# Kernel optimization log

Measured on AMD Instinct MI355X. Metric: run time of the kernel, lower is better.

Reference implementation:

```python
import jax, jax.numpy as jnp
import numpy as np

B, N, ENC, DEC, E, ATT, V, T = 64, 196, 2048, 512, 512, 512, 32000, 32


def setup_inputs() -> dict:
    key = jax.random.key(0)
    ks = jax.random.split(key, 12)
    s = 0.02  # param init scale
    f = lambda k, shape: jax.random.normal(k, shape, jnp.float32) * s
    return {
        "features": jax.random.normal(ks[0], (B, N, ENC), jnp.float32),
        "captions": jax.random.randint(ks[1], (B, T), 0, V),
        "emb": f(ks[2], (V, E)),
        "att_Wenc": f(ks[3], (ENC, ATT)),
        "att_Wdec": f(ks[4], (DEC, ATT)),
        "att_v": f(ks[5], (ATT,)),
        "init_h_W": f(ks[6], (ENC, DEC)), "init_h_b": jnp.zeros((DEC,), jnp.float32),
        "init_c_W": f(ks[7], (ENC, DEC)), "init_c_b": jnp.zeros((DEC,), jnp.float32),
        "W_ih": f(ks[8], (4 * DEC, E + ENC)), "W_hh": f(ks[9], (4 * DEC, DEC)),
        "b_ih": jnp.zeros((4 * DEC,), jnp.float32), "b_hh": jnp.zeros((4 * DEC,), jnp.float32),
        "out_W": f(ks[10], (DEC, V)), "out_b": jnp.zeros((V,), jnp.float32),
    }


def reference(features, captions, emb, att_Wenc, att_Wdec, att_v,
              init_h_W, init_h_b, init_c_W, init_c_b,
              W_ih, W_hh, b_ih, b_hh, out_W, out_b):
    # init hidden/cell from mean-pooled encoder features
    mean_f = features.mean(axis=1)                      # [B, ENC]
    h = mean_f @ init_h_W + init_h_b                    # [B, DEC]
    c = mean_f @ init_c_W + init_c_b                    # [B, DEC]

    enc_att = features @ att_Wenc                       # [B, N, ATT] (loop-invariant)
    embs = emb[captions]                                # [B, T, E]
    xs = jnp.swapaxes(embs[:, :-1], 0, 1)               # [T-1, B, E] time-major

    def step(carry, x):
        h, c = carry
        # Bahdanau attention: tanh(Wf + Wh) . v -> softmax over spatial locations
        e = jnp.tanh(enc_att + (h @ att_Wdec)[:, None, :]) @ att_v   # [B, N]
        alpha = jax.nn.softmax(e, axis=1)                            # [B, N]
        context = jnp.einsum('bn,bnd->bd', alpha, features)          # [B, ENC]
        lstm_in = jnp.concatenate([x, context], axis=1)              # [B, E+ENC]
        gates = lstm_in @ W_ih.T + b_ih + h @ W_hh.T + b_hh          # [B, 4*DEC]
        i, f, g, o = jnp.split(gates, 4, axis=1)                     # torch gate order
        c = jax.nn.sigmoid(f) * c + jax.nn.sigmoid(i) * jnp.tanh(g)
        h = jax.nn.sigmoid(o) * jnp.tanh(c)
        out = h @ out_W + out_b                                      # dropout = identity (eval)
        return (h, c), (out, alpha)

    _, (preds, alphas) = jax.lax.scan(step, (h, c), xs)
    # back to batch-major: preds [B, T-1, V], alphas [B, T-1, N]
    return jnp.swapaxes(preds, 0, 1), jnp.swapaxes(alphas, 0, 1)
```

## Files before the change

kernel.cpp:

```cpp
#include <hip/hip_runtime.h>
#include <math.h>

constexpr int kB = 64, kN = 196, kENC = 2048, kDEC = 512, kE = 512, kATT = 512;
constexpr int kV = 32000, kT = 32, kTS = 31;
constexpr int kKIH = kE + kENC;
constexpr int kKC  = kKIH + kDEC;
constexpr int kG   = 4 * kDEC;
constexpr int kSPL = 8, kKSP = kKC / kSPL;

typedef __attribute__((ext_vector_type(8))) short bf8;
typedef __attribute__((ext_vector_type(4))) float f4;

__device__ __forceinline__ f4 mfma16(bf8 a, bf8 b, f4 c){
  asm("v_mfma_f32_16x16x32_bf16 %0, %1, %2, %0" : "+v"(c) : "v"(a), "v"(b));
  return c;
}
__device__ __forceinline__ float bf2f(unsigned short u){
  return __uint_as_float(((unsigned)u) << 16);
}
__device__ __forceinline__ unsigned short f2b(float f){
  unsigned u = __float_as_uint(f);
  u += 0x7fffu + ((u >> 16) & 1u);
  return (unsigned short)(u >> 16);
}
__device__ __forceinline__ float th_(float x){
  float e2 = __expf(2.f * x);
  return 1.f - 2.f * __builtin_amdgcn_rcpf(e2 + 1.f);
}
__device__ __forceinline__ float sg_(float x){
  return __builtin_amdgcn_rcpf(1.f + __expf(-x));
}

__global__ void k_cvt(const float* __restrict__ src, unsigned short* __restrict__ dst, int n8){
  int i = blockIdx.x * 256 + threadIdx.x;
  if (i >= n8) return;
  float4 a = ((const float4*)src)[2 * i];
  float4 b = ((const float4*)src)[2 * i + 1];
  union { unsigned short u[8]; uint4 v; } t;
  t.u[0] = f2b(a.x); t.u[1] = f2b(a.y); t.u[2] = f2b(a.z); t.u[3] = f2b(a.w);
  t.u[4] = f2b(b.x); t.u[5] = f2b(b.y); t.u[6] = f2b(b.z); t.u[7] = f2b(b.w);
  ((uint4*)dst)[i] = t.v;
}

__global__ __launch_bounds__(256) void k_tcvt(const float* __restrict__ src,
                                              unsigned short* __restrict__ dst, int R, int C){
  __shared__ float t[32][33];
  int c0 = blockIdx.x * 32, r0 = blockIdx.y * 32;
  int tx = threadIdx.x & 31, ty = threadIdx.x >> 5;
  #pragma unroll
  for (int j = 0; j < 4; j++)
    t[ty + 8*j][tx] = src[(size_t)(r0 + ty + 8*j) * C + c0 + tx];
  __syncthreads();
  #pragma unroll
  for (int j = 0; j < 4; j++)
    dst[(size_t)(c0 + ty + 8*j) * R + r0 + tx] = f2b(t[tx][ty + 8*j]);
}

__global__ void k_mean(const float* __restrict__ feat, float* __restrict__ meanf){
  int b = blockIdx.x, d = blockIdx.y * 256 + threadIdx.x;
  const float* p = feat + (size_t)b * kN * kENC + d;
  float s = 0.f;
  for (int n = 0; n < kN; n++) s += p[(size_t)n * kENC];
  meanf[b * kENC + d] = s * (1.f / kN);
}

__global__ __launch_bounds__(512) void k_init(const float* __restrict__ meanf,
                       const float* __restrict__ Wh, const float* __restrict__ bh,
                       const float* __restrict__ Wc, const float* __restrict__ bc,
                       float* __restrict__ h, float* __restrict__ c){
  __shared__ float mf[kENC];
  int b = blockIdx.x;
  for (int i = threadIdx.x; i < kENC; i += 512) mf[i] = meanf[b * kENC + i];
  __syncthreads();
  int j = threadIdx.x;
  const float* W  = blockIdx.y ? Wc : Wh;
  const float* bb = blockIdx.y ? bc : bh;
  float acc = bb[j];
  for (int k = 0; k < kENC; k++) acc = fmaf(mf[k], W[k * kDEC + j], acc);
  (blockIdx.y ? c : h)[b * kDEC + j] = acc;
}

__global__ __launch_bounds__(256) void k_encatt(const unsigned short* __restrict__ A,
                                                const unsigned short* __restrict__ Bt,
                                                unsigned short* __restrict__ Cb){
  int w = threadIdx.x >> 6, lane = threadIdx.x & 63;
  int m0 = blockIdx.x * 128 + w * 32, n0 = blockIdx.y * 64;
  int lr = lane & 15, lk = (lane >> 4) * 8;
  f4 acc[2][4] = {};
  const unsigned short* Ap = A  + (size_t)(m0 + lr) * kENC + lk;
  const unsigned short* Bp = Bt + (size_t)(n0 + lr) * kENC + lk;
  for (int k0 = 0; k0 < kENC; k0 += 32){
    bf8 a0 = *(const bf8*)(Ap + k0);
    bf8 a1 = *(const bf8*)(Ap + 16 * kENC + k0);
    bf8 b0 = *(const bf8*)(Bp + k0);
    bf8 b1 = *(const bf8*)(Bp + 16 * kENC + k0);
    bf8 b2 = *(const bf8*)(Bp + 32 * kENC + k0);
    bf8 b3 = *(const bf8*)(Bp + 48 * kENC + k0);
    acc[0][0] = mfma16(a0, b0, acc[0][0]); acc[0][1] = mfma16(a0, b1, acc[0][1]);
    acc[0][2] = mfma16(a0, b2, acc[0][2]); acc[0][3] = mfma16(a0, b3, acc[0][3]);
    acc[1][0] = mfma16(a1, b0, acc[1][0]); acc[1][1] = mfma16(a1, b1, acc[1][1]);
    acc[1][2] = mfma16(a1, b2, acc[1][2]); acc[1][3] = mfma16(a1, b3, acc[1][3]);
  }
  asm volatile("s_nop 7\n\ts_nop 7");
  int orow = (lane >> 4) * 4;
  #pragma unroll
  for (int mt = 0; mt < 2; mt++)
    #pragma unroll
    for (int nt = 0; nt < 4; nt++)
      #pragma unroll
      for (int r = 0; r < 4; r++)
        Cb[(size_t)(m0 + mt*16 + orow + r) * kATT + n0 + nt*16 + lr] = f2b(acc[mt][nt][r]);
}

__global__ __launch_bounds__(256) void k_e(const unsigned short* __restrict__ EA,
                   const float* __restrict__ hWdec,
                   const float* __restrict__ attv, float* __restrict__ e){
  int w = threadIdx.x >> 6, lane = threadIdx.x & 63;
  int r = blockIdx.x * 4 + w;
  int b = r / kN;
  bf8 ev = *(const bf8*)(EA + (size_t)r * kATT + lane * 8);
  const float* hw = hWdec + b * kATT + lane * 8;
  const float* av = attv + lane * 8;
  float4 h0 = *(const float4*)hw, h1 = *(const float4*)(hw + 4);
  float4 v0 = *(const float4*)av, v1 = *(const float4*)(av + 4);
  float s = 0.f;
  s = fmaf(th_(bf2f((unsigned short)ev[0]) + h0.x), v0.x, s);
  s = fmaf(th_(bf2f((unsigned short)ev[1]) + h0.y), v0.y, s);
  s = fmaf(th_(bf2f((unsigned short)ev[2]) + h0.z), v0.z, s);
  s = fmaf(th_(bf2f((unsigned short)ev[3]) + h0.w), v0.w, s);
  s = fmaf(th_(bf2f((unsigned short)ev[4]) + h1.x), v1.x, s);
  s = fmaf(th_(bf2f((unsigned short)ev[5]) + h1.y), v1.y, s);
  s = fmaf(th_(bf2f((unsigned short)ev[6]) + h1.z), v1.z, s);
  s = fmaf(th_(bf2f((unsigned short)ev[7]) + h1.w), v1.w, s);
  #pragma unroll
  for (int off = 32; off; off >>= 1) s += __shfl_xor(s, off, 64);
  if (lane == 0) e[r] = s;
}

__global__ __launch_bounds__(256) void k_ctx(const float* __restrict__ e,
                     const unsigned short* __restrict__ featb,
                     unsigned short* __restrict__ Xb, float* __restrict__ alphas, int t){
  __shared__ float al[kN];
  __shared__ float red[256];
  int b = blockIdx.x, tid = threadIdx.x;
  float ev = (tid < kN) ? e[b * kN + tid] : -1e30f;
  red[tid] = ev; __syncthreads();
  for (int off = 128; off; off >>= 1){ if (tid < off) red[tid] = fmaxf(red[tid], red[tid + off]); __syncthreads(); }
  float mx = red[0]; __syncthreads();
  float ex = (tid < kN) ? __expf(ev - mx) : 0.f;
  red[tid] = ex; __syncthreads();
  for (int off = 128; off; off >>= 1){ if (tid < off) red[tid] += red[tid + off]; __syncthreads(); }
  float inv = 1.f / red[0];
  if (tid < kN){
    float a = ex * inv;
    al[tid] = a;
    if (blockIdx.y == 0) alphas[((size_t)b * kTS + t) * kN + tid] = a;
  }
  __syncthreads();
  int d = blockIdx.y * 512 + tid * 2;
  const unsigned short* fp = featb + (size_t)b * kN * kENC + d;
  float c0 = 0.f, c1 = 0.f;
  #pragma unroll 4
  for (int n = 0; n < kN; n++){
    unsigned u = *(const unsigned*)(fp + (size_t)n * kENC);
    float a = al[n];
    c0 = fmaf(bf2f((unsigned short)(u & 0xffffu)), a, c0);
    c1 = fmaf(bf2f((unsigned short)(u >> 16)), a, c1);
  }
  unsigned o = ((unsigned)f2b(c1) << 16) | (unsigned)f2b(c0);
  *(unsigned*)(Xb + (size_t)b * kKC + kE + d) = o;
}

__global__ __launch_bounds__(256) void k_gates(const unsigned short* __restrict__ X,
        const unsigned short* __restrict__ Wih, const unsigned short* __restrict__ Whh,
        float* __restrict__ gpart){
  int w = threadIdx.x >> 6, lane = threadIdx.x & 63;
  int n0 = blockIdx.x * 64 + w * 16, ks = blockIdx.y;
  int lr = lane & 15, lk = (lane >> 4) * 8;
  int nrow = n0 + lr;
  f4 acc[4] = {};
  const unsigned short* Xp = X + (size_t)lr * kKC + lk;
  for (int kt = 0; kt < kKSP; kt += 32){
    int kk = ks * kKSP + kt + lk;
    bf8 a0 = *(const bf8*)(Xp + ks * kKSP + kt);
    bf8 a1 = *(const bf8*)(Xp + 16 * kKC + ks * kKSP + kt);
    bf8 a2 = *(const bf8*)(Xp + 32 * kKC + ks * kKSP + kt);
    bf8 a3 = *(const bf8*)(Xp + 48 * kKC + ks * kKSP + kt);
    const unsigned short* bp = (kk < kKIH) ? (Wih + (size_t)nrow * kKIH + kk)
                                           : (Whh + (size_t)nrow * kDEC + (kk - kKIH));
    bf8 b = *(const bf8*)bp;
    acc[0] = mfma16(a0, b, acc[0]); acc[1] = mfma16(a1, b, acc[1]);
    acc[2] = mfma16(a2, b, acc[2]); acc[3] = mfma16(a3, b, acc[3]);
  }
  asm volatile("s_nop 7\n\ts_nop 7");
  float* gp = gpart + (size_t)ks * kB * kG;
  int orow = (lane >> 4) * 4;
  #pragma unroll
  for (int mt = 0; mt < 4; mt++)
    #pragma unroll
    for (int r = 0; r < 4; r++)
      gp[(size_t)(mt*16 + orow + r) * kG + n0 + lr] = acc[mt][r];
}

__global__ __launch_bounds__(512) void k_lstm(const float* __restrict__ gpart,
      const float* __restrict__ bih, const float* __restrict__ bhh,
      float* __restrict__ c, unsigned short* __restrict__ Xb,
      const float* __restrict__ emb, const int* __restrict__ captions,
      const float* __restrict__ Wdec, float* __restrict__ hWdec, int tnext){
  __shared__ float hl[kDEC];
  int b = blockIdx.x, d = threadIdx.x;
  float gi = 0.f, gf = 0.f, gg = 0.f, go = 0.f;
  for (int ks = 0; ks < kSPL; ks++){
    const float* gp = gpart + ((size_t)ks * kB + b) * kG;
    gi += gp[d]; gf += gp[kDEC + d]; gg += gp[2*kDEC + d]; go += gp[3*kDEC + d];
  }
  gi += bih[d]          + bhh[d];
  gf += bih[kDEC + d]   + bhh[kDEC + d];
  gg += bih[2*kDEC + d] + bhh[2*kDEC + d];
  go += bih[3*kDEC + d] + bhh[3*kDEC + d];
  float cn = sg_(gf) * c[b*kDEC + d] + sg_(gi) * th_(gg);
  float hn = sg_(go) * th_(cn);
  c[b*kDEC + d] = cn;
  hl[d] = hn;
  Xb[(size_t)b * kKC + kKIH + d] = f2b(hn);
  Xb[(size_t)b * kKC + d] = f2b(emb[(size_t)captions[b*kT + tnext] * kE + d]);
  __syncthreads();
  float a = 0.f;
  for (int k = 0; k < kDEC; k++) a = fmaf(hl[k], Wdec[(size_t)k * kATT + d], a);
  hWdec[b * kATT + d] = a;
}

__global__ __launch_bounds__(512) void k_prep(const float* __restrict__ h0,
      unsigned short* __restrict__ Xb, const float* __restrict__ emb,
      const int* __restrict__ captions,
      const float* __restrict__ Wdec, float* __restrict__ hWdec){
  __shared__ float hl[kDEC];
  int b = blockIdx.x, d = threadIdx.x;
  float hv = h0[b*kDEC + d];
  hl[d] = hv;
  Xb[(size_t)b * kKC + kKIH + d] = f2b(hv);
  Xb[(size_t)b * kKC + d] = f2b(emb[(size_t)captions[b*kT] * kE + d]);
  __syncthreads();
  float a = 0.f;
  for (int k = 0; k < kDEC; k++) a = fmaf(hl[k], Wdec[(size_t)k * kATT + d], a);
  hWdec[b * kATT + d] = a;
}

__global__ __launch_bounds__(256) void k_out(const unsigned short* __restrict__ Xh,
        const unsigned short* __restrict__ Wt,
        const float* __restrict__ bias, float* __restrict__ preds, int t){
  int w = threadIdx.x >> 6, lane = threadIdx.x & 63;
  int n0 = blockIdx.x * 64 + w * 16;
  int lr = lane & 15, lk = (lane >> 4) * 8;
  float bv = bias[n0 + lr];
  f4 bvv = {bv, bv, bv, bv};
  f4 acc[4] = {bvv, bvv, bvv, bvv};
  const unsigned short* Wp = Wt + (size_t)(n0 + lr) * kDEC + lk;
  const unsigned short* Xp = Xh + (size_t)lr * kKC + lk;
  for (int k0 = 0; k0 < kDEC; k0 += 32){
    bf8 b  = *(const bf8*)(Wp + k0);
    bf8 a0 = *(const bf8*)(Xp + k0);
    bf8 a1 = *(const bf8*)(Xp + 16 * kKC + k0);
    bf8 a2 = *(const bf8*)(Xp + 32 * kKC + k0);
    bf8 a3 = *(const bf8*)(Xp + 48 * kKC + k0);
    acc[0] = mfma16(a0, b, acc[0]); acc[1] = mfma16(a1, b, acc[1]);
    acc[2] = mfma16(a2, b, acc[2]); acc[3] = mfma16(a3, b, acc[3]);
  }
  asm volatile("s_nop 7\n\ts_nop 7");
  int orow = (lane >> 4) * 4;
  #pragma unroll
  for (int mt = 0; mt < 4; mt++)
    #pragma unroll
    for (int r = 0; r < 4; r++){
      int bb = mt*16 + orow + r;
      preds[((size_t)bb * kTS + t) * kV + n0 + lr] = acc[mt][r];
    }
}

extern "C" void kernel_launch(void* const* d_in, const int* in_sizes, int n_in,
                              void* d_out, int out_size, void* d_ws, size_t ws_size,
                              hipStream_t stream) {
  const float* feat     = (const float*)d_in[0];
  const int*   captions = (const int*)  d_in[1];
  const float* emb      = (const float*)d_in[2];
  const float* attWenc  = (const float*)d_in[3];
  const float* attWdec  = (const float*)d_in[4];
  const float* attv     = (const float*)d_in[5];
  const float* ihW      = (const float*)d_in[6];
  const float* ihb      = (const float*)d_in[7];
  const float* icW      = (const float*)d_in[8];
  const float* icb      = (const float*)d_in[9];
  const float* Wih      = (const float*)d_in[10];
  const float* Whh      = (const float*)d_in[11];
  const float* bih      = (const float*)d_in[12];
  const float* bhh      = (const float*)d_in[13];
  const float* outW     = (const float*)d_in[14];
  const float* outb     = (const float*)d_in[15];

  float* preds  = (float*)d_out;
  float* alphas = preds + (size_t)kB * kTS * kV;

  char* p = (char*)d_ws;
  unsigned short* featb  = (unsigned short*)p; p += (size_t)kB*kN*kENC*2;
  unsigned short* outWb  = (unsigned short*)p; p += (size_t)kV*kDEC*2;
  unsigned short* Wihb   = (unsigned short*)p; p += (size_t)kG*kKIH*2;
  unsigned short* Whhb   = (unsigned short*)p; p += (size_t)kG*kDEC*2;
  unsigned short* attWT  = (unsigned short*)p; p += (size_t)kATT*kENC*2;
  unsigned short* encattb= (unsigned short*)p; p += (size_t)kB*kN*kATT*2;
  unsigned short* Xb     = (unsigned short*)p; p += (size_t)kB*kKC*2;
  float* gpart = (float*)p; p += (size_t)kSPL*kB*kG*4;
  float* meanf = (float*)p; p += (size_t)kB*kENC*4;
  float* h0    = (float*)p; p += (size_t)kB*kDEC*4;
  float* cbuf  = (float*)p; p += (size_t)kB*kDEC*4;
  float* hWdec = (float*)p; p += (size_t)kB*kATT*4;
  float* evec  = (float*)p; p += (size_t)kB*kN*4;

  k_cvt<<<(kB*kN*kENC/8 + 255)/256, 256, 0, stream>>>(feat, featb, kB*kN*kENC/8);
  k_cvt<<<(kG*kKIH/8 + 255)/256, 256, 0, stream>>>(Wih, Wihb, kG*kKIH/8);
  k_cvt<<<(kG*kDEC/8 + 255)/256, 256, 0, stream>>>(Whh, Whhb, kG*kDEC/8);
  k_tcvt<<<dim3(kATT/32, kENC/32), 256, 0, stream>>>(attWenc, attWT, kENC, kATT);
  k_tcvt<<<dim3(kV/32, kDEC/32), 256, 0, stream>>>(outW, outWb, kDEC, kV);

  k_mean<<<dim3(kB, kENC/256), 256, 0, stream>>>(feat, meanf);
  k_init<<<dim3(kB, 2), 512, 0, stream>>>(meanf, ihW, ihb, icW, icb, h0, cbuf);
  k_encatt<<<dim3(kB*kN/128, kATT/64), 256, 0, stream>>>(featb, attWT, encattb);
  k_prep<<<kB, 512, 0, stream>>>(h0, Xb, emb, captions, attWdec, hWdec);

  for (int t = 0; t < kTS; ++t) {
    k_e<<<kB*kN/4, 256, 0, stream>>>(encattb, hWdec, attv, evec);
    k_ctx<<<dim3(kB, kENC/512), 256, 0, stream>>>(evec, featb, Xb, alphas, t);
    k_gates<<<dim3(kG/64, kSPL), 256, 0, stream>>>(Xb, Wihb, Whhb, gpart);
    k_lstm<<<kB, 512, 0, stream>>>(gpart, bih, bhh, cbuf, Xb, emb, captions,
                                   attWdec, hWdec, t + 1);
    k_out<<<kV/64, 256, 0, stream>>>(Xb + kKIH, outWb, outb, preds, t);
  }
}
```

Baseline: 2.648 ms.

## Hoist embedding input projection and output projection out of the recurrent loop

Precomputes the embedding half of the LSTM input projection for all timesteps in one batched GEMM. All hidden states are collected into a buffer so the vocabulary projection runs as a single large GEMM after the loop instead of 31 small ones. It also fuses the attention-score and softmax/context kernels into one per-step kernel. This reduces per-step launches and the small-M GEMM inefficiency. In exchange it adds workspace for the gate and hidden-state buffers, stores the precomputed gate term in bf16, and aliases the embedding buffer with the hidden-state buffer.

```diff
diff --git a/kernel.cpp b/kernel.cpp
--- a/kernel.cpp
+++ b/kernel.cpp
@@ -4,9 +4,11 @@
 constexpr int kB = 64, kN = 196, kENC = 2048, kDEC = 512, kE = 512, kATT = 512;
 constexpr int kV = 32000, kT = 32, kTS = 31;
 constexpr int kKIH = kE + kENC;
-constexpr int kKC  = kKIH + kDEC;
+constexpr int kKG  = kENC + kDEC;
 constexpr int kG   = 4 * kDEC;
-constexpr int kSPL = 8, kKSP = kKC / kSPL;
+constexpr int kSPL = 8, kKSP = kKG / kSPL;
+constexpr int kM   = kTS * kB;
+constexpr int kMP  = 2048;
 
 typedef __attribute__((ext_vector_type(8))) short bf8;
 typedef __attribute__((ext_vector_type(4))) float f4;
@@ -80,85 +82,97 @@
   (blockIdx.y ? c : h)[b * kDEC + j] = acc;
 }
 
-__global__ __launch_bounds__(256) void k_encatt(const unsigned short* __restrict__ A,
-                                                const unsigned short* __restrict__ Bt,
-                                                unsigned short* __restrict__ Cb){
+__global__ __launch_bounds__(512) void k_gather(const float* __restrict__ emb,
+        const int* __restrict__ captions, unsigned short* __restrict__ Xemb){
+  int m = blockIdx.x;
+  int t = m >> 6, b = m & 63, d = threadIdx.x;
+  Xemb[(size_t)m * kE + d] = f2b(emb[(size_t)captions[b * kT + t] * kE + d]);
+}
+
+template<int K, int LDA, int LDB, int LDC>
+__global__ __launch_bounds__(256) void k_gemm_nt(const unsigned short* __restrict__ A,
+                                                 const unsigned short* __restrict__ Bt,
+                                                 unsigned short* __restrict__ Cb){
   int w = threadIdx.x >> 6, lane = threadIdx.x & 63;
-  int m0 = blockIdx.x * 128 + w * 32, n0 = blockIdx.y * 64;
+  int m0 = blockIdx.x * 64 + w * 16, n0 = blockIdx.y * 64;
   int lr = lane & 15, lk = (lane >> 4) * 8;
-  f4 acc[2][4] = {};
-  const unsigned short* Ap = A  + (size_t)(m0 + lr) * kENC + lk;
-  const unsigned short* Bp = Bt + (size_t)(n0 + lr) * kENC + lk;
-  for (int k0 = 0; k0 < kENC; k0 += 32){
-    bf8 a0 = *(const bf8*)(Ap + k0);
-    bf8 a1 = *(const bf8*)(Ap + 16 * kENC + k0);
+  f4 acc[4] = {};
+  const unsigned short* Ap = A  + (size_t)(m0 + lr) * LDA + lk;
+  const unsigned short* Bp = Bt + (size_t)(n0 + lr) * LDB + lk;
+  #pragma unroll 4
+  for (int k0 = 0; k0 < K; k0 += 32){
+    bf8 a  = *(const bf8*)(Ap + k0);
     bf8 b0 = *(const bf8*)(Bp + k0);
-    bf8 b1 = *(const bf8*)(Bp + 16 * kENC + k0);
-    bf8 b2 = *(const bf8*)(Bp + 32 * kENC + k0);
-    bf8 b3 = *(const bf8*)(Bp + 48 * kENC + k0);
-    acc[0][0] = mfma16(a0, b0, acc[0][0]); acc[0][1] = mfma16(a0, b1, acc[0][1]);
-    acc[0][2] = mfma16(a0, b2, acc[0][2]); acc[0][3] = mfma16(a0, b3, acc[0][3]);
-    acc[1][0] = mfma16(a1, b0, acc[1][0]); acc[1][1] = mfma16(a1, b1, acc[1][1]);
-    acc[1][2] = mfma16(a1, b2, acc[1][2]); acc[1][3] = mfma16(a1, b3, acc[1][3]);
+    bf8 b1 = *(const bf8*)(Bp + (size_t)16 * LDB + k0);
+    bf8 b2 = *(const bf8*)(Bp + (size_t)32 * LDB + k0);
+    bf8 b3 = *(const bf8*)(Bp + (size_t)48 * LDB + k0);
+    acc[0] = mfma16(a, b0, acc[0]); acc[1] = mfma16(a, b1, acc[1]);
+    acc[2] = mfma16(a, b2, acc[2]); acc[3] = mfma16(a, b3, acc[3]);
   }
   asm volatile("s_nop 7\n\ts_nop 7");
   int orow = (lane >> 4) * 4;
   #pragma unroll
-  for (int mt = 0; mt < 2; mt++)
-    #pragma unroll
-    for (int nt = 0; nt < 4; nt++)
-      #pragma unroll
-      for (int r = 0; r < 4; r++)
-        Cb[(size_t)(m0 + mt*16 + orow + r) * kATT + n0 + nt*16 + lr] = f2b(acc[mt][nt][r]);
-}
-
-__global__ __launch_bounds__(256) void k_e(const unsigned short* __restrict__ EA,
-                   const float* __restrict__ hWdec,
-                   const float* __restrict__ attv, float* __restrict__ e){
-  int w = threadIdx.x >> 6, lane = threadIdx.x & 63;
-  int r = blockIdx.x * 4 + w;
-  int b = r / kN;
-  bf8 ev = *(const bf8*)(EA + (size_t)r * kATT + lane * 8);
-  const float* hw = hWdec + b * kATT + lane * 8;
-  const float* av = attv + lane * 8;
-  float4 h0 = *(const float4*)hw, h1 = *(const float4*)(hw + 4);
-  float4 v0 = *(const float4*)av, v1 = *(const float4*)(av + 4);
-  float s = 0.f;
-  s = fmaf(th_(bf2f((unsigned short)ev[0]) + h0.x), v0.x, s);
-  s = fmaf(th_(bf2f((unsigned short)ev[1]) + h0.y), v0.y, s);
-  s = fmaf(th_(bf2f((unsigned short)ev[2]) + h0.z), v0.z, s);
-  s = fmaf(th_(bf2f((unsigned short)ev[3]) + h0.w), v0.w, s);
-  s = fmaf(th_(bf2f((unsigned short)ev[4]) + h1.x), v1.x, s);
-  s = fmaf(th_(bf2f((unsigned short)ev[5]) + h1.y), v1.y, s);
-  s = fmaf(th_(bf2f((unsigned short)ev[6]) + h1.z), v1.z, s);
-  s = fmaf(th_(bf2f((unsigned short)ev[7]) + h1.w), v1.w, s);
-  #pragma unroll
-  for (int off = 32; off; off >>= 1) s += __shfl_xor(s, off, 64);
-  if (lane == 0) e[r] = s;
-}
-
-__global__ __launch_bounds__(256) void k_ctx(const float* __restrict__ e,
-                     const unsigned short* __restrict__ featb,
-                     unsigned short* __restrict__ Xb, float* __restrict__ alphas, int t){
+  for (int nt = 0; nt < 4; nt++)
+    #pragma unroll
+    for (int r = 0; r < 4; r++)
+      Cb[(size_t)(m0 + orow + r) * LDC + n0 + nt*16 + lr] = f2b(acc[nt][r]);
+}
+
+__global__ __launch_bounds__(512) void k_att(const unsigned short* __restrict__ EA,
+        const float* __restrict__ hWdec, const float* __restrict__ attv,
+        const unsigned short* __restrict__ featb,
+        unsigned short* __restrict__ Xb, float* __restrict__ alphas, int t){
   __shared__ float al[kN];
-  __shared__ float red[256];
-  int b = blockIdx.x, tid = threadIdx.x;
-  float ev = (tid < kN) ? e[b * kN + tid] : -1e30f;
-  red[tid] = ev; __syncthreads();
-  for (int off = 128; off; off >>= 1){ if (tid < off) red[tid] = fmaxf(red[tid], red[tid + off]); __syncthreads(); }
-  float mx = red[0]; __syncthreads();
-  float ex = (tid < kN) ? __expf(ev - mx) : 0.f;
-  red[tid] = ex; __syncthreads();
-  for (int off = 128; off; off >>= 1){ if (tid < off) red[tid] += red[tid + off]; __syncthreads(); }
-  float inv = 1.f / red[0];
-  if (tid < kN){
-    float a = ex * inv;
-    al[tid] = a;
-    if (blockIdx.y == 0) alphas[((size_t)b * kTS + t) * kN + tid] = a;
-  }
-  __syncthreads();
-  int d = blockIdx.y * 512 + tid * 2;
-  const unsigned short* fp = featb + (size_t)b * kN * kENC + d;
+  int b = blockIdx.x, half = blockIdx.y;
+  int tid = threadIdx.x, w = tid >> 6, lane = tid & 63;
+  float hw[8], av[8];
+  {
+    const float* hp = hWdec + b * kATT + lane * 8;
+    const float* ap = attv + lane * 8;
+    #pragma unroll
+    for (int j = 0; j < 8; j++){ hw[j] = hp[j]; av[j] = ap[j]; }
+  }
+  const unsigned short* eb = EA + (size_t)b * kN * kATT;
+  for (int r = w; r < kN; r += 8){
+    bf8 ev = *(const bf8*)(eb + (size_t)r * kATT + lane * 8);
+    float s = 0.f;
+    #pragma unroll
+    for (int j = 0; j < 8; j++)
+      s = fmaf(th_(bf2f((unsigned short)ev[j]) + hw[j]), av[j], s);
+    #pragma unroll
+    for (int off = 32; off; off >>= 1) s += __shfl_xor(s, off, 64);
+    if (lane == 0) al[r] = s;
+  }
+  __syncthreads();
+  if (w == 0){
+    float v[4]; float mx = -1e30f;
+    #pragma unroll
+    for (int i = 0; i < 4; i++){
+      int n = lane + 64 * i;
+      v[i] = (n < kN) ? al[n] : -1e30f;
+      mx = fmaxf(mx, v[i]);
+    }
+    #pragma unroll
+    for (int off = 32; off; off >>= 1) mx = fmaxf(mx, __shfl_xor(mx, off, 64));
+    float sum = 0.f;
+    #pragma unroll
+    for (int i = 0; i < 4; i++){ v[i] = __expf(v[i] - mx); sum += v[i]; }
+    #pragma unroll
+    for (int off = 32; off; off >>= 1) sum += __shfl_xor(sum, off, 64);
+    float inv = 1.f / sum;
+    #pragma unroll
+    for (int i = 0; i < 4; i++){
+      int n = lane + 64 * i;
+      if (n < kN){
+        float a = v[i] * inv;
+        al[n] = a;
+        if (half == 0) alphas[((size_t)b * kTS + t) * kN + n] = a;
+      }
+    }
+  }
+  __syncthreads();
+  int d2 = half * 1024 + tid * 2;
+  const unsigned short* fp = featb + (size_t)b * kN * kENC + d2;
   float c0 = 0.f, c1 = 0.f;
   #pragma unroll 4
   for (int n = 0; n < kN; n++){
@@ -167,8 +181,7 @@
     c0 = fmaf(bf2f((unsigned short)(u & 0xffffu)), a, c0);
     c1 = fmaf(bf2f((unsigned short)(u >> 16)), a, c1);
   }
-  unsigned o = ((unsigned)f2b(c1) << 16) | (unsigned)f2b(c0);
-  *(unsigned*)(Xb + (size_t)b * kKC + kE + d) = o;
+  *(unsigned*)(Xb + (size_t)b * kKG + d2) = ((unsigned)f2b(c1) << 16) | (unsigned)f2b(c0);
 }
 
 __global__ __launch_bounds__(256) void k_gates(const unsigned short* __restrict__ X,
@@ -179,15 +192,16 @@
   int lr = lane & 15, lk = (lane >> 4) * 8;
   int nrow = n0 + lr;
   f4 acc[4] = {};
-  const unsigned short* Xp = X + (size_t)lr * kKC + lk;
+  const unsigned short* Xp = X + (size_t)lr * kKG + ks * kKSP + lk;
+  #pragma unroll 2
   for (int kt = 0; kt < kKSP; kt += 32){
     int kk = ks * kKSP + kt + lk;
-    bf8 a0 = *(const bf8*)(Xp + ks * kKSP + kt);
-    bf8 a1 = *(const bf8*)(Xp + 16 * kKC + ks * kKSP + kt);
-    bf8 a2 = *(const bf8*)(Xp + 32 * kKC + ks * kKSP + kt);
-    bf8 a3 = *(const bf8*)(Xp + 48 * kKC + ks * kKSP + kt);
-    const unsigned short* bp = (kk < kKIH) ? (Wih + (size_t)nrow * kKIH + kk)
-                                           : (Whh + (size_t)nrow * kDEC + (kk - kKIH));
+    bf8 a0 = *(const bf8*)(Xp + kt);
+    bf8 a1 = *(const bf8*)(Xp + 16 * kKG + kt);
+    bf8 a2 = *(const bf8*)(Xp + 32 * kKG + kt);
+    bf8 a3 = *(const bf8*)(Xp + 48 * kKG + kt);
+    const unsigned short* bp = (kk < kENC) ? (Wih + (size_t)nrow * kKIH + kE + kk)
+                                           : (Whh + (size_t)nrow * kDEC + (kk - kENC));
     bf8 b = *(const bf8*)bp;
     acc[0] = mfma16(a0, b, acc[0]); acc[1] = mfma16(a1, b, acc[1]);
     acc[2] = mfma16(a2, b, acc[2]); acc[3] = mfma16(a3, b, acc[3]);
@@ -203,27 +217,31 @@
 }
 
 __global__ __launch_bounds__(512) void k_lstm(const float* __restrict__ gpart,
+      const unsigned short* __restrict__ Gxb,
       const float* __restrict__ bih, const float* __restrict__ bhh,
       float* __restrict__ c, unsigned short* __restrict__ Xb,
-      const float* __restrict__ emb, const int* __restrict__ captions,
-      const float* __restrict__ Wdec, float* __restrict__ hWdec, int tnext){
+      unsigned short* __restrict__ Hall,
+      const float* __restrict__ Wdec, float* __restrict__ hWdec, int t){
   __shared__ float hl[kDEC];
   int b = blockIdx.x, d = threadIdx.x;
+  int m = t * kB + b;
   float gi = 0.f, gf = 0.f, gg = 0.f, go = 0.f;
   for (int ks = 0; ks < kSPL; ks++){
     const float* gp = gpart + ((size_t)ks * kB + b) * kG;
     gi += gp[d]; gf += gp[kDEC + d]; gg += gp[2*kDEC + d]; go += gp[3*kDEC + d];
   }
-  gi += bih[d]          + bhh[d];
-  gf += bih[kDEC + d]   + bhh[kDEC + d];
-  gg += bih[2*kDEC + d] + bhh[2*kDEC + d];
-  go += bih[3*kDEC + d] + bhh[3*kDEC + d];
+  const unsigned short* gx = Gxb + (size_t)m * kG;
+  gi += bf2f(gx[d])          + bih[d]          + bhh[d];
+  gf += bf2f(gx[kDEC + d])   + bih[kDEC + d]   + bhh[kDEC + d];
+  gg += bf2f(gx[2*kDEC + d]) + bih[2*kDEC + d] + bhh[2*kDEC + d];
+  go += bf2f(gx[3*kDEC + d]) + bih[3*kDEC + d] + bhh[3*kDEC + d];
   float cn = sg_(gf) * c[b*kDEC + d] + sg_(gi) * th_(gg);
   float hn = sg_(go) * th_(cn);
   c[b*kDEC + d] = cn;
   hl[d] = hn;
-  Xb[(size_t)b * kKC + kKIH + d] = f2b(hn);
-  Xb[(size_t)b * kKC + d] = f2b(emb[(size_t)captions[b*kT + tnext] * kE + d]);
+  unsigned short hb = f2b(hn);
+  Xb[(size_t)b * kKG + kENC + d] = hb;
+  Hall[(size_t)m * kDEC + d] = hb;
   __syncthreads();
   float a = 0.f;
   for (int k = 0; k < kDEC; k++) a = fmaf(hl[k], Wdec[(size_t)k * kATT + d], a);
@@ -231,49 +249,53 @@
 }
 
 __global__ __launch_bounds__(512) void k_prep(const float* __restrict__ h0,
-      unsigned short* __restrict__ Xb, const float* __restrict__ emb,
-      const int* __restrict__ captions,
+      unsigned short* __restrict__ Xb,
       const float* __restrict__ Wdec, float* __restrict__ hWdec){
   __shared__ float hl[kDEC];
   int b = blockIdx.x, d = threadIdx.x;
   float hv = h0[b*kDEC + d];
   hl[d] = hv;
-  Xb[(size_t)b * kKC + kKIH + d] = f2b(hv);
-  Xb[(size_t)b * kKC + d] = f2b(emb[(size_t)captions[b*kT] * kE + d]);
+  Xb[(size_t)b * kKG + kENC + d] = f2b(hv);
   __syncthreads();
   float a = 0.f;
   for (int k = 0; k < kDEC; k++) a = fmaf(hl[k], Wdec[(size_t)k * kATT + d], a);
   hWdec[b * kATT + d] = a;
 }
 
-__global__ __launch_bounds__(256) void k_out(const unsigned short* __restrict__ Xh,
+__global__ __launch_bounds__(256) void k_bigout(const unsigned short* __restrict__ Hall,
         const unsigned short* __restrict__ Wt,
-        const float* __restrict__ bias, float* __restrict__ preds, int t){
+        const float* __restrict__ bias, float* __restrict__ preds){
   int w = threadIdx.x >> 6, lane = threadIdx.x & 63;
-  int n0 = blockIdx.x * 64 + w * 16;
+  int m0 = blockIdx.x * 64 + w * 16, n0 = blockIdx.y * 128;
   int lr = lane & 15, lk = (lane >> 4) * 8;
-  float bv = bias[n0 + lr];
-  f4 bvv = {bv, bv, bv, bv};
-  f4 acc[4] = {bvv, bvv, bvv, bvv};
-  const unsigned short* Wp = Wt + (size_t)(n0 + lr) * kDEC + lk;
-  const unsigned short* Xp = Xh + (size_t)lr * kKC + lk;
+  f4 acc[8];
+  #pragma unroll
+  for (int nt = 0; nt < 8; nt++){
+    float bv = bias[n0 + nt*16 + lr];
+    acc[nt] = (f4){bv, bv, bv, bv};
+  }
+  const unsigned short* Ap = Hall + (size_t)(m0 + lr) * kDEC + lk;
+  const unsigned short* Bp = Wt + (size_t)(n0 + lr) * kDEC + lk;
+  #pragma unroll 2
   for (int k0 = 0; k0 < kDEC; k0 += 32){
-    bf8 b  = *(const bf8*)(Wp + k0);
-    bf8 a0 = *(const bf8*)(Xp + k0);
-    bf8 a1 = *(const bf8*)(Xp + 16 * kKC + k0);
-    bf8 a2 = *(const bf8*)(Xp + 32 * kKC + k0);
-    bf8 a3 = *(const bf8*)(Xp + 48 * kKC + k0);
-    acc[0] = mfma16(a0, b, acc[0]); acc[1] = mfma16(a1, b, acc[1]);
-    acc[2] = mfma16(a2, b, acc[2]); acc[3] = mfma16(a3, b, acc[3]);
+    bf8 a = *(const bf8*)(Ap + k0);
+    #pragma unroll
+    for (int nt = 0; nt < 8; nt++){
+      bf8 b = *(const bf8*)(Bp + (size_t)nt * 16 * kDEC + k0);
+      acc[nt] = mfma16(a, b, acc[nt]);
+    }
   }
   asm volatile("s_nop 7\n\ts_nop 7");
   int orow = (lane >> 4) * 4;
   #pragma unroll
-  for (int mt = 0; mt < 4; mt++)
+  for (int nt = 0; nt < 8; nt++)
     #pragma unroll
     for (int r = 0; r < 4; r++){
-      int bb = mt*16 + orow + r;
-      preds[((size_t)bb * kTS + t) * kV + n0 + lr] = acc[mt][r];
+      int m = m0 + orow + r;
+      if (m < kM){
+        int t = m >> 6, b = m & 63;
+        preds[((size_t)b * kTS + t) * kV + n0 + nt*16 + lr] = acc[nt][r];
+      }
     }
 }
 
@@ -307,13 +329,15 @@
   unsigned short* Whhb   = (unsigned short*)p; p += (size_t)kG*kDEC*2;
   unsigned short* attWT  = (unsigned short*)p; p += (size_t)kATT*kENC*2;
   unsigned short* encattb= (unsigned short*)p; p += (size_t)kB*kN*kATT*2;
-  unsigned short* Xb     = (unsigned short*)p; p += (size_t)kB*kKC*2;
+  unsigned short* Gxb    = (unsigned short*)p; p += (size_t)kMP*kG*2;
+  unsigned short* Hall   = (unsigned short*)p; p += (size_t)kMP*kDEC*2;
+  unsigned short* Xemb   = Hall;
+  unsigned short* Xb     = (unsigned short*)p; p += (size_t)kB*kKG*2;
   float* gpart = (float*)p; p += (size_t)kSPL*kB*kG*4;
   float* meanf = (float*)p; p += (size_t)kB*kENC*4;
   float* h0    = (float*)p; p += (size_t)kB*kDEC*4;
   float* cbuf  = (float*)p; p += (size_t)kB*kDEC*4;
   float* hWdec = (float*)p; p += (size_t)kB*kATT*4;
-  float* evec  = (float*)p; p += (size_t)kB*kN*4;
 
   k_cvt<<<(kB*kN*kENC/8 + 255)/256, 256, 0, stream>>>(feat, featb, kB*kN*kENC/8);
   k_cvt<<<(kG*kKIH/8 + 255)/256, 256, 0, stream>>>(Wih, Wihb, kG*kKIH/8);
@@ -323,15 +347,20 @@
 
   k_mean<<<dim3(kB, kENC/256), 256, 0, stream>>>(feat, meanf);
   k_init<<<dim3(kB, 2), 512, 0, stream>>>(meanf, ihW, ihb, icW, icb, h0, cbuf);
-  k_encatt<<<dim3(kB*kN/128, kATT/64), 256, 0, stream>>>(featb, attWT, encattb);
-  k_prep<<<kB, 512, 0, stream>>>(h0, Xb, emb, captions, attWdec, hWdec);
+
+  k_gather<<<kM, 512, 0, stream>>>(emb, captions, Xemb);
+  k_gemm_nt<kE, kE, kKIH, kG><<<dim3(kMP/64, kG/64), 256, 0, stream>>>(Xemb, Wihb, Gxb);
+
+  k_gemm_nt<kENC, kENC, kENC, kATT><<<dim3(kB*kN/64, kATT/64), 256, 0, stream>>>(featb, attWT, encattb);
+
+  k_prep<<<kB, 512, 0, stream>>>(h0, Xb, attWdec, hWdec);
 
   for (int t = 0; t < kTS; ++t) {
-    k_e<<<kB*kN/4, 256, 0, stream>>>(encattb, hWdec, attv, evec);
-    k_ctx<<<dim3(kB, kENC/512), 256, 0, stream>>>(evec, featb, Xb, alphas, t);
+    k_att<<<dim3(kB, 2), 512, 0, stream>>>(encattb, hWdec, attv, featb, Xb, alphas, t);
     k_gates<<<dim3(kG/64, kSPL), 256, 0, stream>>>(Xb, Wihb, Whhb, gpart);
-    k_lstm<<<kB, 512, 0, stream>>>(gpart, bih, bhh, cbuf, Xb, emb, captions,
-                                   attWdec, hWdec, t + 1);
-    k_out<<<kV/64, 256, 0, stream>>>(Xb + kKIH, outWb, outb, preds, t);
-  }
-}
+    k_lstm<<<kB, 512, 0, stream>>>(gpart, Gxb, bih, bhh, cbuf, Xb, Hall,
+                                   attWdec, hWdec, t);
+  }
+
+  k_bigout<<<dim3(kMP/64, kV/128), 256, 0, stream>>>(Hall, outWb, outb, preds);
+}
```

After: 2.902 ms. 1.1x slower.
